# Optimization experiments

Measured on AMD Instinct MI355X. Metric: run time of the kernel, lower is better.

Reference implementation:

```python
import jax, jax.numpy as jnp
import numpy as np

B, S, C, V, LAT, NL = 256, 512, 256, 32, 256, 7
DILS = [1, 2, 4, 8, 16, 32, 64]
EPS = 1e-5


def setup_inputs() -> dict:
    key = jax.random.key(0)
    ks = jax.random.split(key, 24)
    s = 0.05
    inp = {
        "x": jax.random.randint(ks[0], (B, S), 0, V, dtype=jnp.int64 if jax.config.read("jax_enable_x64") else jnp.int32),
        "z": jax.random.normal(ks[1], (B, LAT), dtype=jnp.float32),
        "emb": jax.random.normal(ks[2], (V, C), dtype=jnp.float32) * s,
        "latent_W": jax.random.normal(ks[3], (LAT, C), dtype=jnp.float32) * s,
        "latent_b": jnp.zeros((C,), jnp.float32),
        "ln1_g": jnp.ones((NL, C), jnp.float32),
        "ln1_b": jnp.zeros((NL, C), jnp.float32),
        "w1": jax.random.normal(ks[4], (NL, C, C), jnp.float32) * s,
        "b1": jnp.zeros((NL, C), jnp.float32),
        "ln2_g": jnp.ones((NL, C), jnp.float32),
        "ln2_b": jnp.zeros((NL, C), jnp.float32),
        "wd": jax.random.normal(ks[5], (NL, 2, C, C), jnp.float32) * s,  # tap 0 = x[t-d], tap 1 = x[t]
        "bd": jnp.zeros((NL, C), jnp.float32),
        "ln3_g": jnp.ones((NL, C), jnp.float32),
        "ln3_b": jnp.zeros((NL, C), jnp.float32),
        "we": jax.random.normal(ks[6], (NL, C, C), jnp.float32) * s,
        "be": jnp.zeros((NL, C), jnp.float32),
        "wg": jax.random.normal(ks[7], (NL, C, C), jnp.float32) * s,
        "bg": jnp.zeros((NL, C), jnp.float32),
        "out_W": jax.random.normal(ks[8], (C, V), jnp.float32) * s,
        "out_b": jnp.zeros((V,), jnp.float32),
    }
    return inp


def _ln(h, g, b):
    mu = h.mean(-1, keepdims=True)
    var = jnp.mean((h - mu) ** 2, axis=-1, keepdims=True)
    return (h - mu) * jax.lax.rsqrt(var + EPS) * g + b


def _lrelu(h):
    return jnp.where(h >= 0, h, 0.01 * h)


def reference(x, z, emb, latent_W, latent_b, ln1_g, ln1_b, w1, b1,
              ln2_g, ln2_b, wd, bd, ln3_g, ln3_b, we, be, wg, bg,
              out_W, out_b):
    # channel-last layout [B, S, C] throughout (fuses away the torch transposes)
    h = emb[x] + (z @ latent_W + latent_b)[:, None, :]
    for i, d in enumerate(DILS):
        x_inp = h
        t = _lrelu(_ln(x_inp, ln1_g[i], ln1_b[i]))
        t = t @ w1[i] + b1[i]
        t = _lrelu(_ln(t, ln2_g[i], ln2_b[i]))
        # causal dilated conv, kernel=2: out[t] = W0*x[t-d] + W1*x[t]
        t_shift = jnp.pad(t, ((0, 0), (d, 0), (0, 0)))[:, :t.shape[1], :]
        t = t_shift @ wd[i, 0] + t @ wd[i, 1] + bd[i]
        t = _lrelu(_ln(t, ln3_g[i], ln3_b[i]))
        gated = (t @ we[i] + be[i]) * jax.nn.sigmoid(t @ wg[i] + bg[i])
        h = gated + x_inp
    logits = h @ out_W + out_b                      # [B, S, V]
    lp = jax.nn.log_softmax(logits, axis=-1)
    # gather log-prob of next token: lp[:, :-1, :] at x[:, 1:]
    return jnp.take_along_axis(lp[:, :-1, :], x[:, 1:, None], axis=2)[..., 0]
```

## Files before the change

kernel.cpp:

```cpp
#include <hip/hip_runtime.h>

typedef unsigned short u16;
typedef unsigned int   u32;
typedef __attribute__((ext_vector_type(8))) short short8;
typedef __attribute__((ext_vector_type(4))) float f32x4;

struct __align__(8) u16x4 { u16 x, y, z, w; };

#define NL 7
#define M_DIM 131072

__device__ __forceinline__ float b2f(u16 u) {
  union { float f; u32 i; } c; c.i = ((u32)u) << 16; return c.f;
}
__device__ __forceinline__ u16 f2b(float f) {
  union { float f; u32 i; } c; c.f = f;
  u32 r = c.i + 0x7FFFu + ((c.i >> 16) & 1u);
  return (u16)(r >> 16);
}
__device__ __forceinline__ float wave_sum(float v) {
  #pragma unroll
  for (int off = 1; off < 64; off <<= 1) v += __shfl_xor(v, off);
  return v;
}
__device__ __forceinline__ void gload16(const void* g, void* l) {
  __builtin_amdgcn_global_load_lds((const __attribute__((address_space(1))) void*)g,
                                   (__attribute__((address_space(3))) void*)l, 16, 0, 0);
}


__global__ __launch_bounds__(256) void conv_w1_k(const float* __restrict__ w1, u16* __restrict__ wT) {
  int idx = blockIdx.x * 256 + threadIdx.x;
  int i = idx >> 16, rem = idx & 65535;
  int n = rem >> 8, k = rem & 255;
  wT[idx] = f2b(w1[(i << 16) + (k << 8) + n]);
}

__global__ __launch_bounds__(256) void conv_wd_k(const float* __restrict__ wd, u16* __restrict__ wT) {
  int idx = blockIdx.x * 256 + threadIdx.x;
  int i = idx / 131072, rem = idx & 131071;
  int n = rem >> 9, k2 = rem & 511;
  int tap = k2 >> 8, k = k2 & 255;
  wT[idx] = f2b(wd[(((i * 2 + tap) << 8) + k) * 256 + n]);
}

__global__ __launch_bounds__(256) void conv_weg_k(const float* __restrict__ we, const float* __restrict__ wg,
                                                  u16* __restrict__ wT) {
  int idx = blockIdx.x * 256 + threadIdx.x;
  int i = idx / 131072, rem = idx & 131071;
  int src = rem >> 16, n = (rem >> 8) & 255, k = rem & 255;
  const float* W = src ? wg : we;
  wT[idx] = f2b(W[((i << 8) + k) * 256 + n]);
}

__global__ __launch_bounds__(256) void conv_wo_k(const float* __restrict__ outW, u16* __restrict__ wTo) {
  int idx = blockIdx.x * 256 + threadIdx.x;
  int v = idx >> 8, k = idx & 255;
  wTo[idx] = f2b(outW[k * 32 + v]);
}


__global__ __launch_bounds__(256) void zlat_k(const float* __restrict__ z, const float* __restrict__ W,
                                              const float* __restrict__ bias, float* __restrict__ zlat) {
  int b = blockIdx.x, c = threadIdx.x;
  float acc = bias[c];
  for (int l = 0; l < 256; ++l) acc += z[b * 256 + l] * W[l * 256 + c];
  zlat[b * 256 + c] = acc;
}


__device__ __forceinline__ void ln_lrelu4(float v0, float v1, float v2, float v3,
                                          const float* __restrict__ g, const float* __restrict__ b,
                                          int c, u16x4* out) {
  float s = wave_sum(v0 + v1 + v2 + v3);
  float q = wave_sum(v0 * v0 + v1 * v1 + v2 * v2 + v3 * v3);
  float mu = s * 0.00390625f;
  float var = q * 0.00390625f - mu * mu;
  float rs = rsqrtf(var + 1e-5f);
  float4 gv = *(const float4*)&g[c];
  float4 bv = *(const float4*)&b[c];
  float y0 = (v0 - mu) * rs * gv.x + bv.x; y0 = y0 >= 0.f ? y0 : 0.01f * y0;
  float y1 = (v1 - mu) * rs * gv.y + bv.y; y1 = y1 >= 0.f ? y1 : 0.01f * y1;
  float y2 = (v2 - mu) * rs * gv.z + bv.z; y2 = y2 >= 0.f ? y2 : 0.01f * y2;
  float y3 = (v3 - mu) * rs * gv.w + bv.w; y3 = y3 >= 0.f ? y3 : 0.01f * y3;
  out->x = f2b(y0); out->y = f2b(y1); out->z = f2b(y2); out->w = f2b(y3);
}


__global__ __launch_bounds__(256) void embed_ln_k(const int* __restrict__ x, const float* __restrict__ emb,
                                                  const float* __restrict__ zlat,
                                                  const float* __restrict__ g, const float* __restrict__ b,
                                                  u16* __restrict__ h, u16* __restrict__ tOut) {
  int wave = threadIdx.x >> 6, lane = threadIdx.x & 63;
  int r = blockIdx.x * 4 + wave;
  int c = lane * 4;
  int tok = x[r];
  int bi = r >> 9;
  float4 ev = *(const float4*)&emb[tok * 256 + c];
  float4 zv = *(const float4*)&zlat[bi * 256 + c];
  float v0 = ev.x + zv.x, v1 = ev.y + zv.y, v2 = ev.z + zv.z, v3 = ev.w + zv.w;
  u16x4 hb; hb.x = f2b(v0); hb.y = f2b(v1); hb.z = f2b(v2); hb.w = f2b(v3);
  *(u16x4*)&h[(long)r * 256 + c] = hb;
  u16x4 ov;
  ln_lrelu4(v0, v1, v2, v3, g, b, c, &ov);
  *(u16x4*)&tOut[(long)r * 256 + c] = ov;
}


__global__ __launch_bounds__(256) void gemm_ln_k(
    const u16* __restrict__ A, const u16* __restrict__ WT, int Ktot, int dil,
    const float* __restrict__ bias, const float* __restrict__ g, const float* __restrict__ b,
    u16* __restrict__ Out)
{
  __shared__ u16 lA[64 * 32];
  __shared__ u16 lB[256 * 32];
  __shared__ float pS[64][4], pQ[64][4];
  __shared__ float muA[64], rsA[64];
  const int tid = threadIdx.x;
  const int lane = tid & 63;
  const int wv = tid >> 6;
  const int wc = wv * 64;
  const int m0 = blockIdx.x * 64;
  const int rA = tid >> 2;
  const int cA = (tid & 3) * 8;
  const int mm = m0 + rA;
  const int s1 = mm & 511;
  const bool fixBlk = (dil > 0) && ((m0 & 511) < dil);

  f32x4 acc[4][4];
  #pragma unroll
  for (int i = 0; i < 4; ++i)
    #pragma unroll
    for (int j = 0; j < 4; ++j) {
      acc[i][j][0] = 0.f; acc[i][j][1] = 0.f; acc[i][j][2] = 0.f; acc[i][j][3] = 0.f;
    }

  const int nkt = Ktot >> 5;
  for (int kt = 0; kt < nkt; ++kt) {
    const int kk = (kt & 7) * 32;
    int r = mm;
    if (dil > 0 && kt < 8) r = (s1 >= dil) ? (mm - dil) : mm;
    gload16(A + (long)r * 256 + kk + cA, &lA[rA * 32 + cA]);
    const u16* bSrc = WT + (long)rA * Ktot + kt * 32 + cA;
    #pragma unroll
    for (int j = 0; j < 4; ++j)
      gload16(bSrc + (long)(64 * j) * Ktot, &lB[(rA + 64 * j) * 32 + cA]);
    __syncthreads();

    if (fixBlk && kt < 8) {
      if (rA < dil) {
        uint4 zz; zz.x = 0; zz.y = 0; zz.z = 0; zz.w = 0;
        *(uint4*)&lA[rA * 32 + cA] = zz;
      }
      __syncthreads();
    }

    const int lq = (lane >> 4) * 8;
    const int lr = lane & 15;
    short8 af[4], bfr[4];
    #pragma unroll
    for (int mt = 0; mt < 4; ++mt)
      af[mt] = *(const short8*)&lA[(mt * 16 + lr) * 32 + lq];
    #pragma unroll
    for (int nt = 0; nt < 4; ++nt)
      bfr[nt] = *(const short8*)&lB[(wc + nt * 16 + lr) * 32 + lq];
    #pragma unroll
    for (int mt = 0; mt < 4; ++mt)
      #pragma unroll
      for (int nt = 0; nt < 4; ++nt)
        acc[mt][nt] = __builtin_amdgcn_mfma_f32_16x16x32_bf16(af[mt], bfr[nt], acc[mt][nt], 0, 0, 0);
    __syncthreads();
  }

  const int lr = lane & 15;
  const int quad = lane >> 4;
  float biasv[4], gv[4], bv[4];
  #pragma unroll
  for (int nt = 0; nt < 4; ++nt) {
    int n = wc + nt * 16 + lr;
    biasv[nt] = bias[n]; gv[nt] = g[n]; bv[nt] = b[n];
  }
  #pragma unroll
  for (int mt = 0; mt < 4; ++mt)
    #pragma unroll
    for (int r = 0; r < 4; ++r) {
      float s = 0.f, q = 0.f;
      #pragma unroll
      for (int nt = 0; nt < 4; ++nt) {
        float v = acc[mt][nt][r] + biasv[nt];
        acc[mt][nt][r] = v;
        s += v; q += v * v;
      }
      #pragma unroll
      for (int off = 1; off < 16; off <<= 1) {
        s += __shfl_xor(s, off); q += __shfl_xor(q, off);
      }
      if (lr == 0) { pS[mt * 16 + quad * 4 + r][wv] = s; pQ[mt * 16 + quad * 4 + r][wv] = q; }
    }
  __syncthreads();
  if (tid < 64) {
    float S = pS[tid][0] + pS[tid][1] + pS[tid][2] + pS[tid][3];
    float Q = pQ[tid][0] + pQ[tid][1] + pQ[tid][2] + pQ[tid][3];
    float mu = S * 0.00390625f;
    float var = Q * 0.00390625f - mu * mu;
    muA[tid] = mu; rsA[tid] = rsqrtf(var + 1e-5f);
  }
  __syncthreads();
  #pragma unroll
  for (int mt = 0; mt < 4; ++mt)
    #pragma unroll
    for (int r = 0; r < 4; ++r) {
      int row = mt * 16 + quad * 4 + r;
      float mu = muA[row], rs = rsA[row];
      #pragma unroll
      for (int nt = 0; nt < 4; ++nt) {
        float y = (acc[mt][nt][r] - mu) * rs * gv[nt] + bv[nt];
        y = y >= 0.f ? y : 0.01f * y;
        Out[(long)(m0 + row) * 256 + wc + nt * 16 + lr] = f2b(y);
      }
    }
}


__global__ __launch_bounds__(256, 2) void gemm_gate_ln_k(
    const u16* __restrict__ P, const u16* __restrict__ WTe, const u16* __restrict__ WTg,
    const float* __restrict__ be, const float* __restrict__ bg,
    const float* __restrict__ g, const float* __restrict__ b,
    u16* __restrict__ h, u16* __restrict__ tOut, int doLN)
{
  __shared__ u16 lA[64 * 32];
  __shared__ u16 lBe[256 * 32];
  __shared__ u16 lBg[256 * 32];
  __shared__ float pS[64][4], pQ[64][4];
  __shared__ float muA[64], rsA[64];
  const int tid = threadIdx.x;
  const int lane = tid & 63;
  const int wv = tid >> 6;
  const int wc = wv * 64;
  const int m0 = blockIdx.x * 64;
  const int rA = tid >> 2;
  const int cA = (tid & 3) * 8;

  f32x4 accE[4][4], accG[4][4];
  #pragma unroll
  for (int i = 0; i < 4; ++i)
    #pragma unroll
    for (int j = 0; j < 4; ++j) {
      accE[i][j][0] = 0.f; accE[i][j][1] = 0.f; accE[i][j][2] = 0.f; accE[i][j][3] = 0.f;
      accG[i][j][0] = 0.f; accG[i][j][1] = 0.f; accG[i][j][2] = 0.f; accG[i][j][3] = 0.f;
    }

  for (int kt = 0; kt < 8; ++kt) {
    const int kk = kt * 32;
    gload16(P + (long)(m0 + rA) * 256 + kk + cA, &lA[rA * 32 + cA]);
    const long bofs = (long)rA * 256 + kk + cA;
    #pragma unroll
    for (int j = 0; j < 4; ++j) {
      gload16(WTe + bofs + (long)(64 * j) * 256, &lBe[(rA + 64 * j) * 32 + cA]);
      gload16(WTg + bofs + (long)(64 * j) * 256, &lBg[(rA + 64 * j) * 32 + cA]);
    }
    __syncthreads();

    const int lq = (lane >> 4) * 8;
    const int lr = lane & 15;
    short8 af[4], bfe[4], bfg[4];
    #pragma unroll
    for (int mt = 0; mt < 4; ++mt)
      af[mt] = *(const short8*)&lA[(mt * 16 + lr) * 32 + lq];
    #pragma unroll
    for (int nt = 0; nt < 4; ++nt) {
      bfe[nt] = *(const short8*)&lBe[(wc + nt * 16 + lr) * 32 + lq];
      bfg[nt] = *(const short8*)&lBg[(wc + nt * 16 + lr) * 32 + lq];
    }
    #pragma unroll
    for (int mt = 0; mt < 4; ++mt)
      #pragma unroll
      for (int nt = 0; nt < 4; ++nt) {
        accE[mt][nt] = __builtin_amdgcn_mfma_f32_16x16x32_bf16(af[mt], bfe[nt], accE[mt][nt], 0, 0, 0);
        accG[mt][nt] = __builtin_amdgcn_mfma_f32_16x16x32_bf16(af[mt], bfg[nt], accG[mt][nt], 0, 0, 0);
      }
    __syncthreads();
  }

  const int lr = lane & 15;
  const int quad = lane >> 4;
  float bev[4], bgv[4];
  #pragma unroll
  for (int nt = 0; nt < 4; ++nt) {
    int n = wc + nt * 16 + lr;
    bev[nt] = be[n]; bgv[nt] = bg[n];
  }
  #pragma unroll
  for (int mt = 0; mt < 4; ++mt)
    #pragma unroll
    for (int r = 0; r < 4; ++r) {
      int row = mt * 16 + quad * 4 + r;
      long off = (long)(m0 + row) * 256;
      float s = 0.f, q = 0.f;
      #pragma unroll
      for (int nt = 0; nt < 4; ++nt) {
        int n = wc + nt * 16 + lr;
        float e = accE[mt][nt][r] + bev[nt];
        float gg = accG[mt][nt][r] + bgv[nt];
        float hv = b2f(h[off + n]);
        float hn = e * (1.f / (1.f + expf(-gg))) + hv;
        h[off + n] = f2b(hn);
        accE[mt][nt][r] = hn;
        s += hn; q += hn * hn;
      }
      #pragma unroll
      for (int off2 = 1; off2 < 16; off2 <<= 1) {
        s += __shfl_xor(s, off2); q += __shfl_xor(q, off2);
      }
      if (lr == 0) { pS[row][wv] = s; pQ[row][wv] = q; }
    }
  __syncthreads();
  if (tid < 64) {
    float S = pS[tid][0] + pS[tid][1] + pS[tid][2] + pS[tid][3];
    float Q = pQ[tid][0] + pQ[tid][1] + pQ[tid][2] + pQ[tid][3];
    float mu = S * 0.00390625f;
    float var = Q * 0.00390625f - mu * mu;
    muA[tid] = mu; rsA[tid] = rsqrtf(var + 1e-5f);
  }
  __syncthreads();
  if (doLN) {
    float gv[4], bv[4];
    #pragma unroll
    for (int nt = 0; nt < 4; ++nt) {
      int n = wc + nt * 16 + lr;
      gv[nt] = g[n]; bv[nt] = b[n];
    }
    #pragma unroll
    for (int mt = 0; mt < 4; ++mt)
      #pragma unroll
      for (int r = 0; r < 4; ++r) {
        int row = mt * 16 + quad * 4 + r;
        float mu = muA[row], rs = rsA[row];
        #pragma unroll
        for (int nt = 0; nt < 4; ++nt) {
          float y = (accE[mt][nt][r] - mu) * rs * gv[nt] + bv[nt];
          y = y >= 0.f ? y : 0.01f * y;
          tOut[(long)(m0 + row) * 256 + wc + nt * 16 + lr] = f2b(y);
        }
      }
  }
}


__global__ __launch_bounds__(256) void final_k(const u16* __restrict__ h, const u16* __restrict__ WTo,
                                               const float* __restrict__ outb, const int* __restrict__ x,
                                               float* __restrict__ out) {
  __shared__ u16 lW[32 * 264];
  const int tid = threadIdx.x;
  const int lane = tid & 63;
  const int wv = tid >> 6;
  const int mBase = blockIdx.x * 256 + wv * 64;

  #pragma unroll
  for (int j = 0; j < 4; ++j) {
    int chunk = tid + 256 * j;
    int v = chunk >> 5, k8 = chunk & 31;
    uint4 w4 = *(const uint4*)(WTo + v * 256 + k8 * 8);
    *(uint4*)&lW[v * 264 + k8 * 8] = w4;
  }
  __syncthreads();

  const int lq = (lane >> 4) * 8;
  const int lr = lane & 15;
  const int quad = lane >> 4;

  f32x4 acc[4][2];
  #pragma unroll
  for (int mt = 0; mt < 4; ++mt) {
    acc[mt][0][0] = 0.f; acc[mt][0][1] = 0.f; acc[mt][0][2] = 0.f; acc[mt][0][3] = 0.f;
    acc[mt][1][0] = 0.f; acc[mt][1][1] = 0.f; acc[mt][1][2] = 0.f; acc[mt][1][3] = 0.f;
  }

  for (int kt = 0; kt < 8; ++kt) {
    short8 bf0 = *(const short8*)&lW[lr * 264 + kt * 32 + lq];
    short8 bf1 = *(const short8*)&lW[(16 + lr) * 264 + kt * 32 + lq];
    #pragma unroll
    for (int mt = 0; mt < 4; ++mt) {
      short8 af = *(const short8*)(h + (long)(mBase + mt * 16 + lr) * 256 + kt * 32 + lq);
      acc[mt][0] = __builtin_amdgcn_mfma_f32_16x16x32_bf16(af, bf0, acc[mt][0], 0, 0, 0);
      acc[mt][1] = __builtin_amdgcn_mfma_f32_16x16x32_bf16(af, bf1, acc[mt][1], 0, 0, 0);
    }
  }

  float ob0 = outb[lr], ob1 = outb[16 + lr];
  #pragma unroll
  for (int mt = 0; mt < 4; ++mt)
    #pragma unroll
    for (int r = 0; r < 4; ++r) {
      int row = mBase + mt * 16 + quad * 4 + r;
      float lo = acc[mt][0][r] + ob0;
      float hi = acc[mt][1][r] + ob1;
      float mx = fmaxf(lo, hi);
      #pragma unroll
      for (int o = 1; o < 16; o <<= 1) mx = fmaxf(mx, __shfl_xor(mx, o));
      float se = expf(lo - mx) + expf(hi - mx);
      #pragma unroll
      for (int o = 1; o < 16; o <<= 1) se += __shfl_xor(se, o);
      int s = row & 511;
      int xa = (s == 511) ? row : (row + 1);
      int tok = x[xa];
      float lg = (tok < 16) ? lo : hi;
      float lp = lg - mx - logf(se);
      if (s != 511 && lr == (tok & 15))
        out[(row >> 9) * 511 + s] = lp;
    }
}


extern "C" void kernel_launch(void* const* d_in, const int* in_sizes, int n_in,
                              void* d_out, int out_size, void* d_ws, size_t ws_size,
                              hipStream_t stream) {
  const int*   x    = (const int*)d_in[0];
  const float* z    = (const float*)d_in[1];
  const float* emb  = (const float*)d_in[2];
  const float* latW = (const float*)d_in[3];
  const float* latb = (const float*)d_in[4];
  const float* ln1g = (const float*)d_in[5];
  const float* ln1b = (const float*)d_in[6];
  const float* w1   = (const float*)d_in[7];
  const float* b1   = (const float*)d_in[8];
  const float* ln2g = (const float*)d_in[9];
  const float* ln2b = (const float*)d_in[10];
  const float* wd   = (const float*)d_in[11];
  const float* bd   = (const float*)d_in[12];
  const float* ln3g = (const float*)d_in[13];
  const float* ln3b = (const float*)d_in[14];
  const float* we   = (const float*)d_in[15];
  const float* be   = (const float*)d_in[16];
  const float* wg   = (const float*)d_in[17];
  const float* bg   = (const float*)d_in[18];
  const float* outW = (const float*)d_in[19];
  const float* outb = (const float*)d_in[20];

  char* ws = (char*)d_ws;
  u16*   h    = (u16*)(ws + 0);
  u16*   bufA = (u16*)(ws + 67108864);
  u16*   bufB = (u16*)(ws + 134217728);
  float* zlat = (float*)(ws + 201326592);
  u16*   wT1  = (u16*)(ws + 201588736);
  u16*   wTd  = (u16*)(ws + 202506240);
  u16*   wTeg = (u16*)(ws + 204341248);
  u16*   wTo  = (u16*)(ws + 206176256);

  conv_w1_k <<<1792, 256, 0, stream>>>(w1, wT1);
  conv_wd_k <<<3584, 256, 0, stream>>>(wd, wTd);
  conv_weg_k<<<3584, 256, 0, stream>>>(we, wg, wTeg);
  conv_wo_k <<<32, 256, 0, stream>>>(outW, wTo);
  zlat_k    <<<256, 256, 0, stream>>>(z, latW, latb, zlat);
  embed_ln_k<<<M_DIM / 4, 256, 0, stream>>>(x, emb, zlat, ln1g, ln1b, h, bufA);

  u16* X = bufA;
  u16* Y = bufB;
  for (int i = 0; i < NL; ++i) {
    int d = 1 << i;
    int doLN = (i < NL - 1) ? 1 : 0;
    int ni = doLN ? (i + 1) : i;
    gemm_ln_k<<<M_DIM / 64, 256, 0, stream>>>(
        X, wT1 + i * 65536, 256, 0, b1 + i * 256, ln2g + i * 256, ln2b + i * 256, Y);
    gemm_ln_k<<<M_DIM / 64, 256, 0, stream>>>(
        Y, wTd + i * 131072, 512, d, bd + i * 256, ln3g + i * 256, ln3b + i * 256, X);
    gemm_gate_ln_k<<<M_DIM / 64, 256, 0, stream>>>(
        X, wTeg + i * 131072, wTeg + i * 131072 + 65536, be + i * 256, bg + i * 256,
        ln1g + ni * 256, ln1b + ni * 256, h, Y, doLN);
    u16* tmp = X; X = Y; Y = tmp;
  }

  final_k<<<M_DIM / 256, 256, 0, stream>>>(h, wTo, outb, x, (float*)d_out);
}
```

Before: 1.693 ms.

## Restructure layer kernels into persistent weight-resident GEMMs with separate LayerNorm passes

After: 2.801 ms. +65.5%, slower.

```diff
diff --git a/kernel.cpp b/kernel.cpp
--- a/kernel.cpp
+++ b/kernel.cpp
@@ -17,15 +17,6 @@
   union { float f; u32 i; } c; c.f = f;
   u32 r = c.i + 0x7FFFu + ((c.i >> 16) & 1u);
   return (u16)(r >> 16);
-}
-__device__ __forceinline__ float wave_sum(float v) {
-  #pragma unroll
-  for (int off = 1; off < 64; off <<= 1) v += __shfl_xor(v, off);
-  return v;
-}
-__device__ __forceinline__ void gload16(const void* g, void* l) {
-  __builtin_amdgcn_global_load_lds((const __attribute__((address_space(1))) void*)g,
-                                   (__attribute__((address_space(3))) void*)l, 16, 0, 0);
 }
 
 
@@ -69,11 +60,34 @@
 }
 
 
-__device__ __forceinline__ void ln_lrelu4(float v0, float v1, float v2, float v3,
-                                          const float* __restrict__ g, const float* __restrict__ b,
-                                          int c, u16x4* out) {
-  float s = wave_sum(v0 + v1 + v2 + v3);
-  float q = wave_sum(v0 * v0 + v1 * v1 + v2 * v2 + v3 * v3);
+__global__ __launch_bounds__(256) void embed_k(const int* __restrict__ x, const float* __restrict__ emb,
+                                               const float* __restrict__ zlat, u16* __restrict__ h) {
+  int wave = threadIdx.x >> 6, lane = threadIdx.x & 63;
+  int r = blockIdx.x * 4 + wave;
+  int c = lane * 4;
+  int tok = x[r];
+  int bi = r >> 9;
+  float4 ev = *(const float4*)&emb[tok * 256 + c];
+  float4 zv = *(const float4*)&zlat[bi * 256 + c];
+  u16x4 hb;
+  hb.x = f2b(ev.x + zv.x); hb.y = f2b(ev.y + zv.y);
+  hb.z = f2b(ev.z + zv.z); hb.w = f2b(ev.w + zv.w);
+  *(u16x4*)&h[(long)r * 256 + c] = hb;
+}
+
+
+__global__ __launch_bounds__(256) void ln_act_k(const u16* __restrict__ in,
+                                                const float* __restrict__ g, const float* __restrict__ b,
+                                                u16* __restrict__ out) {
+  int wave = threadIdx.x >> 6, lane = threadIdx.x & 63;
+  int r = blockIdx.x * 4 + wave;
+  int c = lane * 4;
+  u16x4 iv = *(const u16x4*)&in[(long)r * 256 + c];
+  float v0 = b2f(iv.x), v1 = b2f(iv.y), v2 = b2f(iv.z), v3 = b2f(iv.w);
+  float s = v0 + v1 + v2 + v3;
+  float q = v0 * v0 + v1 * v1 + v2 * v2 + v3 * v3;
+  #pragma unroll
+  for (int o = 1; o < 64; o <<= 1) { s += __shfl_xor(s, o); q += __shfl_xor(q, o); }
   float mu = s * 0.00390625f;
   float var = q * 0.00390625f - mu * mu;
   float rs = rsqrtf(var + 1e-5f);
@@ -83,266 +97,265 @@
   float y1 = (v1 - mu) * rs * gv.y + bv.y; y1 = y1 >= 0.f ? y1 : 0.01f * y1;
   float y2 = (v2 - mu) * rs * gv.z + bv.z; y2 = y2 >= 0.f ? y2 : 0.01f * y2;
   float y3 = (v3 - mu) * rs * gv.w + bv.w; y3 = y3 >= 0.f ? y3 : 0.01f * y3;
-  out->x = f2b(y0); out->y = f2b(y1); out->z = f2b(y2); out->w = f2b(y3);
-}
-
-
-__global__ __launch_bounds__(256) void embed_ln_k(const int* __restrict__ x, const float* __restrict__ emb,
-                                                  const float* __restrict__ zlat,
-                                                  const float* __restrict__ g, const float* __restrict__ b,
-                                                  u16* __restrict__ h, u16* __restrict__ tOut) {
-  int wave = threadIdx.x >> 6, lane = threadIdx.x & 63;
-  int r = blockIdx.x * 4 + wave;
-  int c = lane * 4;
-  int tok = x[r];
-  int bi = r >> 9;
-  float4 ev = *(const float4*)&emb[tok * 256 + c];
-  float4 zv = *(const float4*)&zlat[bi * 256 + c];
-  float v0 = ev.x + zv.x, v1 = ev.y + zv.y, v2 = ev.z + zv.z, v3 = ev.w + zv.w;
-  u16x4 hb; hb.x = f2b(v0); hb.y = f2b(v1); hb.z = f2b(v2); hb.w = f2b(v3);
-  *(u16x4*)&h[(long)r * 256 + c] = hb;
-  u16x4 ov;
-  ln_lrelu4(v0, v1, v2, v3, g, b, c, &ov);
-  *(u16x4*)&tOut[(long)r * 256 + c] = ov;
-}
-
-
-__global__ __launch_bounds__(256) void gemm_ln_k(
-    const u16* __restrict__ A, const u16* __restrict__ WT, int Ktot, int dil,
-    const float* __restrict__ bias, const float* __restrict__ g, const float* __restrict__ b,
-    u16* __restrict__ Out)
+  u16x4 ov; ov.x = f2b(y0); ov.y = f2b(y1); ov.z = f2b(y2); ov.w = f2b(y3);
+  *(u16x4*)&out[(long)r * 256 + c] = ov;
+}
+
+
+__global__ __launch_bounds__(256) void gemm1_k(
+    const u16* __restrict__ h, const u16* __restrict__ WT,
+    const float* __restrict__ lng, const float* __restrict__ lnb,
+    const float* __restrict__ bias, u16* __restrict__ U)
 {
-  __shared__ u16 lA[64 * 32];
-  __shared__ u16 lB[256 * 32];
-  __shared__ float pS[64][4], pQ[64][4];
-  __shared__ float muA[64], rsA[64];
+  __shared__ __align__(16) u16 lA[128 * 264];
+  __shared__ __align__(16) u16 lB[128 * 264];
   const int tid = threadIdx.x;
   const int lane = tid & 63;
   const int wv = tid >> 6;
-  const int wc = wv * 64;
-  const int m0 = blockIdx.x * 64;
-  const int rA = tid >> 2;
-  const int cA = (tid & 3) * 8;
-  const int mm = m0 + rA;
-  const int s1 = mm & 511;
-  const bool fixBlk = (dil > 0) && ((m0 & 511) < dil);
-
-  f32x4 acc[4][4];
-  #pragma unroll
-  for (int i = 0; i < 4; ++i)
-    #pragma unroll
-    for (int j = 0; j < 4; ++j) {
-      acc[i][j][0] = 0.f; acc[i][j][1] = 0.f; acc[i][j][2] = 0.f; acc[i][j][3] = 0.f;
-    }
-
-  const int nkt = Ktot >> 5;
-  for (int kt = 0; kt < nkt; ++kt) {
-    const int kk = (kt & 7) * 32;
-    int r = mm;
-    if (dil > 0 && kt < 8) r = (s1 >= dil) ? (mm - dil) : mm;
-    gload16(A + (long)r * 256 + kk + cA, &lA[rA * 32 + cA]);
-    const u16* bSrc = WT + (long)rA * Ktot + kt * 32 + cA;
-    #pragma unroll
-    for (int j = 0; j < 4; ++j)
-      gload16(bSrc + (long)(64 * j) * Ktot, &lB[(rA + 64 * j) * 32 + cA]);
+  const int mw = wv >> 1, nw = wv & 1;
+  const int lr = lane & 15, quad = lane >> 4, lq = quad * 8;
+  const int ng = blockIdx.x & 1;
+  const int mb = blockIdx.x >> 1;
+
+  #pragma unroll
+  for (int jj = 0; jj < 16; ++jj) {
+    int c = tid + 256 * jj;
+    int row = c >> 5, c8 = c & 31;
+    *(uint4*)&lB[row * 264 + c8 * 8] = *(const uint4*)(WT + (long)(ng * 128 + row) * 256 + c8 * 8);
+  }
+
+  const int half = lane >> 5, l5 = lane & 31;
+  float4 ga = *(const float4*)&lng[l5 * 8];
+  float4 gb = *(const float4*)&lng[l5 * 8 + 4];
+  float4 ba = *(const float4*)&lnb[l5 * 8];
+  float4 bb = *(const float4*)&lnb[l5 * 8 + 4];
+  float biasv[4];
+  #pragma unroll
+  for (int nt = 0; nt < 4; ++nt) biasv[nt] = bias[ng * 128 + nw * 64 + nt * 16 + lr];
+
+  for (int j = 0; j < 4; ++j) {
+    const int m0 = (mb + j * 256) * 128;
     __syncthreads();
-
-    if (fixBlk && kt < 8) {
-      if (rA < dil) {
-        uint4 zz; zz.x = 0; zz.y = 0; zz.z = 0; zz.w = 0;
-        *(uint4*)&lA[rA * 32 + cA] = zz;
+    #pragma unroll 4
+    for (int it = 0; it < 16; ++it) {
+      int row = wv * 32 + it * 2 + half;
+      uint4 hv = *(const uint4*)(h + (long)(m0 + row) * 256 + l5 * 8);
+      float v0 = b2f((u16)(hv.x & 0xffff)), v1 = b2f((u16)(hv.x >> 16));
+      float v2 = b2f((u16)(hv.y & 0xffff)), v3 = b2f((u16)(hv.y >> 16));
+      float v4 = b2f((u16)(hv.z & 0xffff)), v5 = b2f((u16)(hv.z >> 16));
+      float v6 = b2f((u16)(hv.w & 0xffff)), v7 = b2f((u16)(hv.w >> 16));
+      float s = v0 + v1 + v2 + v3 + v4 + v5 + v6 + v7;
+      float q = v0*v0 + v1*v1 + v2*v2 + v3*v3 + v4*v4 + v5*v5 + v6*v6 + v7*v7;
+      #pragma unroll
+      for (int o = 1; o < 32; o <<= 1) { s += __shfl_xor(s, o); q += __shfl_xor(q, o); }
+      float mu = s * 0.00390625f;
+      float var = q * 0.00390625f - mu * mu;
+      float rs = rsqrtf(var + 1e-5f);
+      float y0 = (v0 - mu) * rs * ga.x + ba.x; y0 = y0 >= 0.f ? y0 : 0.01f * y0;
+      float y1 = (v1 - mu) * rs * ga.y + ba.y; y1 = y1 >= 0.f ? y1 : 0.01f * y1;
+      float y2 = (v2 - mu) * rs * ga.z + ba.z; y2 = y2 >= 0.f ? y2 : 0.01f * y2;
+      float y3 = (v3 - mu) * rs * ga.w + ba.w; y3 = y3 >= 0.f ? y3 : 0.01f * y3;
+      float y4 = (v4 - mu) * rs * gb.x + bb.x; y4 = y4 >= 0.f ? y4 : 0.01f * y4;
+      float y5 = (v5 - mu) * rs * gb.y + bb.y; y5 = y5 >= 0.f ? y5 : 0.01f * y5;
+      float y6 = (v6 - mu) * rs * gb.z + bb.z; y6 = y6 >= 0.f ? y6 : 0.01f * y6;
+      float y7 = (v7 - mu) * rs * gb.w + bb.w; y7 = y7 >= 0.f ? y7 : 0.01f * y7;
+      uint4 ov;
+      ov.x = (u32)f2b(y0) | ((u32)f2b(y1) << 16);
+      ov.y = (u32)f2b(y2) | ((u32)f2b(y3) << 16);
+      ov.z = (u32)f2b(y4) | ((u32)f2b(y5) << 16);
+      ov.w = (u32)f2b(y6) | ((u32)f2b(y7) << 16);
+      *(uint4*)&lA[row * 264 + l5 * 8] = ov;
+    }
+    __syncthreads();
+
+    f32x4 acc[4][4];
+    #pragma unroll
+    for (int a = 0; a < 4; ++a)
+      #pragma unroll
+      for (int bq = 0; bq < 4; ++bq) { acc[a][bq][0]=0.f; acc[a][bq][1]=0.f; acc[a][bq][2]=0.f; acc[a][bq][3]=0.f; }
+
+    #pragma unroll
+    for (int kt = 0; kt < 8; ++kt) {
+      short8 af[4], bf[4];
+      #pragma unroll
+      for (int mt = 0; mt < 4; ++mt)
+        af[mt] = *(const short8*)&lA[(mw * 64 + mt * 16 + lr) * 264 + kt * 32 + lq];
+      #pragma unroll
+      for (int nt = 0; nt < 4; ++nt)
+        bf[nt] = *(const short8*)&lB[(nw * 64 + nt * 16 + lr) * 264 + kt * 32 + lq];
+      #pragma unroll
+      for (int mt = 0; mt < 4; ++mt)
+        #pragma unroll
+        for (int nt = 0; nt < 4; ++nt)
+          acc[mt][nt] = __builtin_amdgcn_mfma_f32_16x16x32_bf16(af[mt], bf[nt], acc[mt][nt], 0, 0, 0);
+    }
+
+    #pragma unroll
+    for (int mt = 0; mt < 4; ++mt)
+      #pragma unroll
+      for (int r = 0; r < 4; ++r) {
+        int m = m0 + mw * 64 + mt * 16 + quad * 4 + r;
+        #pragma unroll
+        for (int nt = 0; nt < 4; ++nt)
+          U[(long)m * 256 + ng * 128 + nw * 64 + nt * 16 + lr] = f2b(acc[mt][nt][r] + biasv[nt]);
       }
-      __syncthreads();
-    }
-
-    const int lq = (lane >> 4) * 8;
-    const int lr = lane & 15;
-    short8 af[4], bfr[4];
-    #pragma unroll
-    for (int mt = 0; mt < 4; ++mt)
-      af[mt] = *(const short8*)&lA[(mt * 16 + lr) * 32 + lq];
-    #pragma unroll
-    for (int nt = 0; nt < 4; ++nt)
-      bfr[nt] = *(const short8*)&lB[(wc + nt * 16 + lr) * 32 + lq];
-    #pragma unroll
-    for (int mt = 0; mt < 4; ++mt)
-      #pragma unroll
-      for (int nt = 0; nt < 4; ++nt)
-        acc[mt][nt] = __builtin_amdgcn_mfma_f32_16x16x32_bf16(af[mt], bfr[nt], acc[mt][nt], 0, 0, 0);
-    __syncthreads();
-  }
-
-  const int lr = lane & 15;
-  const int quad = lane >> 4;
-  float biasv[4], gv[4], bv[4];
-  #pragma unroll
-  for (int nt = 0; nt < 4; ++nt) {
-    int n = wc + nt * 16 + lr;
-    biasv[nt] = bias[n]; gv[nt] = g[n]; bv[nt] = b[n];
-  }
-  #pragma unroll
-  for (int mt = 0; mt < 4; ++mt)
-    #pragma unroll
-    for (int r = 0; r < 4; ++r) {
-      float s = 0.f, q = 0.f;
-      #pragma unroll
-      for (int nt = 0; nt < 4; ++nt) {
-        float v = acc[mt][nt][r] + biasv[nt];
-        acc[mt][nt][r] = v;
-        s += v; q += v * v;
-      }
-      #pragma unroll
-      for (int off = 1; off < 16; off <<= 1) {
-        s += __shfl_xor(s, off); q += __shfl_xor(q, off);
-      }
-      if (lr == 0) { pS[mt * 16 + quad * 4 + r][wv] = s; pQ[mt * 16 + quad * 4 + r][wv] = q; }
-    }
-  __syncthreads();
-  if (tid < 64) {
-    float S = pS[tid][0] + pS[tid][1] + pS[tid][2] + pS[tid][3];
-    float Q = pQ[tid][0] + pQ[tid][1] + pQ[tid][2] + pQ[tid][3];
-    float mu = S * 0.00390625f;
-    float var = Q * 0.00390625f - mu * mu;
-    muA[tid] = mu; rsA[tid] = rsqrtf(var + 1e-5f);
-  }
-  __syncthreads();
-  #pragma unroll
-  for (int mt = 0; mt < 4; ++mt)
-    #pragma unroll
-    for (int r = 0; r < 4; ++r) {
-      int row = mt * 16 + quad * 4 + r;
-      float mu = muA[row], rs = rsA[row];
-      #pragma unroll
-      for (int nt = 0; nt < 4; ++nt) {
-        float y = (acc[mt][nt][r] - mu) * rs * gv[nt] + bv[nt];
-        y = y >= 0.f ? y : 0.01f * y;
-        Out[(long)(m0 + row) * 256 + wc + nt * 16 + lr] = f2b(y);
-      }
-    }
-}
-
-
-__global__ __launch_bounds__(256, 2) void gemm_gate_ln_k(
-    const u16* __restrict__ P, const u16* __restrict__ WTe, const u16* __restrict__ WTg,
-    const float* __restrict__ be, const float* __restrict__ bg,
-    const float* __restrict__ g, const float* __restrict__ b,
-    u16* __restrict__ h, u16* __restrict__ tOut, int doLN)
+  }
+}
+
+
+__global__ __launch_bounds__(256) void dil_k(
+    const u16* __restrict__ V, const u16* __restrict__ WT, int dil,
+    const float* __restrict__ bias, u16* __restrict__ W)
 {
-  __shared__ u16 lA[64 * 32];
-  __shared__ u16 lBe[256 * 32];
-  __shared__ u16 lBg[256 * 32];
-  __shared__ float pS[64][4], pQ[64][4];
-  __shared__ float muA[64], rsA[64];
+  __shared__ __align__(16) u16 lB[128 * 520];
   const int tid = threadIdx.x;
   const int lane = tid & 63;
   const int wv = tid >> 6;
-  const int wc = wv * 64;
-  const int m0 = blockIdx.x * 64;
-  const int rA = tid >> 2;
-  const int cA = (tid & 3) * 8;
-
-  f32x4 accE[4][4], accG[4][4];
-  #pragma unroll
-  for (int i = 0; i < 4; ++i)
-    #pragma unroll
-    for (int j = 0; j < 4; ++j) {
-      accE[i][j][0] = 0.f; accE[i][j][1] = 0.f; accE[i][j][2] = 0.f; accE[i][j][3] = 0.f;
-      accG[i][j][0] = 0.f; accG[i][j][1] = 0.f; accG[i][j][2] = 0.f; accG[i][j][3] = 0.f;
-    }
-
-  for (int kt = 0; kt < 8; ++kt) {
-    const int kk = kt * 32;
-    gload16(P + (long)(m0 + rA) * 256 + kk + cA, &lA[rA * 32 + cA]);
-    const long bofs = (long)rA * 256 + kk + cA;
-    #pragma unroll
-    for (int j = 0; j < 4; ++j) {
-      gload16(WTe + bofs + (long)(64 * j) * 256, &lBe[(rA + 64 * j) * 32 + cA]);
-      gload16(WTg + bofs + (long)(64 * j) * 256, &lBg[(rA + 64 * j) * 32 + cA]);
-    }
+  const int mw = wv >> 1, nw = wv & 1;
+  const int lr = lane & 15, quad = lane >> 4, lq = quad * 8;
+  const int ng = blockIdx.x & 1;
+  const int mb = blockIdx.x >> 1;
+
+  #pragma unroll
+  for (int jj = 0; jj < 32; ++jj) {
+    int c = tid + 256 * jj;
+    int row = c >> 6, c8 = c & 63;
+    *(uint4*)&lB[row * 520 + c8 * 8] = *(const uint4*)(WT + (long)(ng * 128 + row) * 512 + c8 * 8);
+  }
+  float biasv[4];
+  #pragma unroll
+  for (int nt = 0; nt < 4; ++nt) biasv[nt] = bias[ng * 128 + nw * 64 + nt * 16 + lr];
+  __syncthreads();
+
+  const short8 zfrag = {0, 0, 0, 0, 0, 0, 0, 0};
+  for (int j = 0; j < 4; ++j) {
+    const int m0 = (mb + j * 256) * 128;
+    f32x4 acc[4][4];
+    #pragma unroll
+    for (int a = 0; a < 4; ++a)
+      #pragma unroll
+      for (int bq = 0; bq < 4; ++bq) { acc[a][bq][0]=0.f; acc[a][bq][1]=0.f; acc[a][bq][2]=0.f; acc[a][bq][3]=0.f; }
+
+    #pragma unroll 4
+    for (int kt = 0; kt < 16; ++kt) {
+      const int kk = (kt & 7) * 32;
+      const bool tap0 = (kt < 8);
+      short8 af[4], bf[4];
+      #pragma unroll
+      for (int mt = 0; mt < 4; ++mt) {
+        int m = m0 + mw * 64 + mt * 16 + lr;
+        int s = m & 511;
+        int r = (tap0 && s >= dil) ? (m - dil) : m;
+        af[mt] = *(const short8*)(V + (long)r * 256 + kk + lq);
+        if (tap0 && s < dil) af[mt] = zfrag;
+      }
+      #pragma unroll
+      for (int nt = 0; nt < 4; ++nt)
+        bf[nt] = *(const short8*)&lB[(nw * 64 + nt * 16 + lr) * 520 + kt * 32 + lq];
+      #pragma unroll
+      for (int mt = 0; mt < 4; ++mt)
+        #pragma unroll
+        for (int nt = 0; nt < 4; ++nt)
+          acc[mt][nt] = __builtin_amdgcn_mfma_f32_16x16x32_bf16(af[mt], bf[nt], acc[mt][nt], 0, 0, 0);
+    }
+
+    #pragma unroll
+    for (int mt = 0; mt < 4; ++mt)
+      #pragma unroll
+      for (int r = 0; r < 4; ++r) {
+        int m = m0 + mw * 64 + mt * 16 + quad * 4 + r;
+        #pragma unroll
+        for (int nt = 0; nt < 4; ++nt)
+          W[(long)m * 256 + ng * 128 + nw * 64 + nt * 16 + lr] = f2b(acc[mt][nt][r] + biasv[nt]);
+      }
+  }
+}
+
+
+__global__ __launch_bounds__(256) void gate_k(
+    const u16* __restrict__ P, const u16* __restrict__ WTe, const u16* __restrict__ WTg,
+    const float* __restrict__ be, const float* __restrict__ bg, u16* __restrict__ h)
+{
+  __shared__ __align__(16) u16 lBe[64 * 264];
+  __shared__ __align__(16) u16 lBg[64 * 264];
+  __shared__ float xch[2 * 64 * 65];
+  const int tid = threadIdx.x;
+  const int lane = tid & 63;
+  const int wv = tid >> 6;
+  const int mw = wv >> 1, sg = wv & 1;
+  const int lr = lane & 15, quad = lane >> 4, lq = quad * 8;
+  const int ng = blockIdx.x & 3;
+  const int mb = blockIdx.x >> 2;
+
+  #pragma unroll
+  for (int jj = 0; jj < 8; ++jj) {
+    int c = tid + 256 * jj;
+    int row = c >> 5, c8 = c & 31;
+    *(uint4*)&lBe[row * 264 + c8 * 8] = *(const uint4*)(WTe + (long)(ng * 64 + row) * 256 + c8 * 8);
+    *(uint4*)&lBg[row * 264 + c8 * 8] = *(const uint4*)(WTg + (long)(ng * 64 + row) * 256 + c8 * 8);
+  }
+  const u16* lB = sg ? lBg : lBe;
+  const float* bsrc = sg ? bg : be;
+  float biasv[4];
+  #pragma unroll
+  for (int nt = 0; nt < 4; ++nt) biasv[nt] = bsrc[ng * 64 + nt * 16 + lr];
+  __syncthreads();
+
+  for (int j = 0; j < 8; ++j) {
+    const int m0 = (mb + j * 128) * 128;
+    f32x4 acc[4][4];
+    #pragma unroll
+    for (int a = 0; a < 4; ++a)
+      #pragma unroll
+      for (int bq = 0; bq < 4; ++bq) { acc[a][bq][0]=0.f; acc[a][bq][1]=0.f; acc[a][bq][2]=0.f; acc[a][bq][3]=0.f; }
+
+    #pragma unroll 4
+    for (int kt = 0; kt < 8; ++kt) {
+      short8 af[4], bf[4];
+      #pragma unroll
+      for (int mt = 0; mt < 4; ++mt)
+        af[mt] = *(const short8*)(P + (long)(m0 + mw * 64 + mt * 16 + lr) * 256 + kt * 32 + lq);
+      #pragma unroll
+      for (int nt = 0; nt < 4; ++nt)
+        bf[nt] = *(const short8*)&lB[(nt * 16 + lr) * 264 + kt * 32 + lq];
+      #pragma unroll
+      for (int mt = 0; mt < 4; ++mt)
+        #pragma unroll
+        for (int nt = 0; nt < 4; ++nt)
+          acc[mt][nt] = __builtin_amdgcn_mfma_f32_16x16x32_bf16(af[mt], bf[nt], acc[mt][nt], 0, 0, 0);
+    }
+
     __syncthreads();
-
-    const int lq = (lane >> 4) * 8;
-    const int lr = lane & 15;
-    short8 af[4], bfe[4], bfg[4];
-    #pragma unroll
-    for (int mt = 0; mt < 4; ++mt)
-      af[mt] = *(const short8*)&lA[(mt * 16 + lr) * 32 + lq];
-    #pragma unroll
-    for (int nt = 0; nt < 4; ++nt) {
-      bfe[nt] = *(const short8*)&lBe[(wc + nt * 16 + lr) * 32 + lq];
-      bfg[nt] = *(const short8*)&lBg[(wc + nt * 16 + lr) * 32 + lq];
-    }
-    #pragma unroll
-    for (int mt = 0; mt < 4; ++mt)
-      #pragma unroll
-      for (int nt = 0; nt < 4; ++nt) {
-        accE[mt][nt] = __builtin_amdgcn_mfma_f32_16x16x32_bf16(af[mt], bfe[nt], accE[mt][nt], 0, 0, 0);
-        accG[mt][nt] = __builtin_amdgcn_mfma_f32_16x16x32_bf16(af[mt], bfg[nt], accG[mt][nt], 0, 0, 0);
-      }
+    if (sg) {
+      #pragma unroll
+      for (int mt = 0; mt < 4; ++mt)
+        #pragma unroll
+        for (int r = 0; r < 4; ++r) {
+          int row = mt * 16 + quad * 4 + r;
+          #pragma unroll
+          for (int nt = 0; nt < 4; ++nt) {
+            float g = acc[mt][nt][r] + biasv[nt];
+            xch[(mw * 64 + row) * 65 + nt * 16 + lr] = 1.f / (1.f + expf(-g));
+          }
+        }
+    }
     __syncthreads();
-  }
-
-  const int lr = lane & 15;
-  const int quad = lane >> 4;
-  float bev[4], bgv[4];
-  #pragma unroll
-  for (int nt = 0; nt < 4; ++nt) {
-    int n = wc + nt * 16 + lr;
-    bev[nt] = be[n]; bgv[nt] = bg[n];
-  }
-  #pragma unroll
-  for (int mt = 0; mt < 4; ++mt)
-    #pragma unroll
-    for (int r = 0; r < 4; ++r) {
-      int row = mt * 16 + quad * 4 + r;
-      long off = (long)(m0 + row) * 256;
-      float s = 0.f, q = 0.f;
-      #pragma unroll
-      for (int nt = 0; nt < 4; ++nt) {
-        int n = wc + nt * 16 + lr;
-        float e = accE[mt][nt][r] + bev[nt];
-        float gg = accG[mt][nt][r] + bgv[nt];
-        float hv = b2f(h[off + n]);
-        float hn = e * (1.f / (1.f + expf(-gg))) + hv;
-        h[off + n] = f2b(hn);
-        accE[mt][nt][r] = hn;
-        s += hn; q += hn * hn;
-      }
-      #pragma unroll
-      for (int off2 = 1; off2 < 16; off2 <<= 1) {
-        s += __shfl_xor(s, off2); q += __shfl_xor(q, off2);
-      }
-      if (lr == 0) { pS[row][wv] = s; pQ[row][wv] = q; }
-    }
-  __syncthreads();
-  if (tid < 64) {
-    float S = pS[tid][0] + pS[tid][1] + pS[tid][2] + pS[tid][3];
-    float Q = pQ[tid][0] + pQ[tid][1] + pQ[tid][2] + pQ[tid][3];
-    float mu = S * 0.00390625f;
-    float var = Q * 0.00390625f - mu * mu;
-    muA[tid] = mu; rsA[tid] = rsqrtf(var + 1e-5f);
-  }
-  __syncthreads();
-  if (doLN) {
-    float gv[4], bv[4];
-    #pragma unroll
-    for (int nt = 0; nt < 4; ++nt) {
-      int n = wc + nt * 16 + lr;
-      gv[nt] = g[n]; bv[nt] = b[n];
-    }
-    #pragma unroll
-    for (int mt = 0; mt < 4; ++mt)
-      #pragma unroll
-      for (int r = 0; r < 4; ++r) {
-        int row = mt * 16 + quad * 4 + r;
-        float mu = muA[row], rs = rsA[row];
-        #pragma unroll
-        for (int nt = 0; nt < 4; ++nt) {
-          float y = (accE[mt][nt][r] - mu) * rs * gv[nt] + bv[nt];
-          y = y >= 0.f ? y : 0.01f * y;
-          tOut[(long)(m0 + row) * 256 + wc + nt * 16 + lr] = f2b(y);
+    if (!sg) {
+      #pragma unroll
+      for (int mt = 0; mt < 4; ++mt)
+        #pragma unroll
+        for (int r = 0; r < 4; ++r) {
+          int row = mt * 16 + quad * 4 + r;
+          long off = (long)(m0 + mw * 64 + row) * 256 + ng * 64;
+          #pragma unroll
+          for (int nt = 0; nt < 4; ++nt) {
+            int n = nt * 16 + lr;
+            float e = acc[mt][nt][r] + biasv[nt];
+            float sgm = xch[(mw * 64 + row) * 65 + n];
+            h[off + n] = f2b(e * sgm + b2f(h[off + n]));
+          }
         }
-      }
+    }
   }
 }
 
@@ -372,8 +385,8 @@
   f32x4 acc[4][2];
   #pragma unroll
   for (int mt = 0; mt < 4; ++mt) {
-    acc[mt][0][0] = 0.f; acc[mt][0][1] = 0.f; acc[mt][0][2] = 0.f; acc[mt][0][3] = 0.f;
-    acc[mt][1][0] = 0.f; acc[mt][1][1] = 0.f; acc[mt][1][2] = 0.f; acc[mt][1][3] = 0.f;
+    acc[mt][0][0]=0.f; acc[mt][0][1]=0.f; acc[mt][0][2]=0.f; acc[mt][0][3]=0.f;
+    acc[mt][1][0]=0.f; acc[mt][1][1]=0.f; acc[mt][1][2]=0.f; acc[mt][1][3]=0.f;
   }
 
   for (int kt = 0; kt < 8; ++kt) {
@@ -452,22 +465,17 @@
   conv_weg_k<<<3584, 256, 0, stream>>>(we, wg, wTeg);
   conv_wo_k <<<32, 256, 0, stream>>>(outW, wTo);
   zlat_k    <<<256, 256, 0, stream>>>(z, latW, latb, zlat);
-  embed_ln_k<<<M_DIM / 4, 256, 0, stream>>>(x, emb, zlat, ln1g, ln1b, h, bufA);
-
-  u16* X = bufA;
-  u16* Y = bufB;
+  embed_k   <<<M_DIM / 4, 256, 0, stream>>>(x, emb, zlat, h);
+
   for (int i = 0; i < NL; ++i) {
     int d = 1 << i;
-    int doLN = (i < NL - 1) ? 1 : 0;
-    int ni = doLN ? (i + 1) : i;
-    gemm_ln_k<<<M_DIM / 64, 256, 0, stream>>>(
-        X, wT1 + i * 65536, 256, 0, b1 + i * 256, ln2g + i * 256, ln2b + i * 256, Y);
-    gemm_ln_k<<<M_DIM / 64, 256, 0, stream>>>(
-        Y, wTd + i * 131072, 512, d, bd + i * 256, ln3g + i * 256, ln3b + i * 256, X);
-    gemm_gate_ln_k<<<M_DIM / 64, 256, 0, stream>>>(
-        X, wTeg + i * 131072, wTeg + i * 131072 + 65536, be + i * 256, bg + i * 256,
-        ln1g + ni * 256, ln1b + ni * 256, h, Y, doLN);
-    u16* tmp = X; X = Y; Y = tmp;
+    gemm1_k<<<512, 256, 0, stream>>>(h, wT1 + i * 65536, ln1g + i * 256, ln1b + i * 256,
+                                     b1 + i * 256, bufB);
+    ln_act_k<<<M_DIM / 4, 256, 0, stream>>>(bufB, ln2g + i * 256, ln2b + i * 256, bufA);
+    dil_k<<<512, 256, 0, stream>>>(bufA, wTd + i * 131072, d, bd + i * 256, bufB);
+    ln_act_k<<<M_DIM / 4, 256, 0, stream>>>(bufB, ln3g + i * 256, ln3b + i * 256, bufA);
+    gate_k<<<512, 256, 0, stream>>>(bufA, wTeg + i * 131072, wTeg + i * 131072 + 65536,
+                                    be + i * 256, bg + i * 256, h);
   }
 
   final_k<<<M_DIM / 256, 256, 0, stream>>>(h, wTo, outb, x, (float*)d_out);
```
